# Kernel tuning notes

Measured on AMD Instinct MI355X. Metric: run time of the kernel, lower is better.

Reference implementation:

```python
import jax, jax.numpy as jnp
import numpy as np

B, T, E = 8, 2048, 1024  # batch, seq_len, emb_size (= output_emb_size)


def setup_inputs() -> dict:
    key = jax.random.key(0)
    k1, k2, k3, k4, k5, k6, k7 = jax.random.split(key, 7)
    return {
        "q": jax.random.normal(k1, (B, T, E), jnp.float32),
        "k": jax.random.normal(k2, (B, T, E), jnp.float32),
        "v": jax.random.normal(k3, (B, T, E), jnp.float32),
        "mask": jax.random.randint(k4, (T, T), 0, 2, jnp.int32),
        # nn.Linear weights, stored [out, in] as in torch; applied as x @ W.T
        "Wq": jax.random.normal(k5, (E, E), jnp.float32) / np.sqrt(E),
        "Wk": jax.random.normal(k6, (E, E), jnp.float32) / np.sqrt(E),
        "Wv": jax.random.normal(k7, (E, E), jnp.float32) / np.sqrt(E),
    }


def reference(q, k, v, mask, Wq, Wk, Wv):
    # QKV projections (bias-free Linear): x @ W.T
    query = jnp.einsum("bte,oe->bto", q, Wq)
    key_p = jnp.einsum("bse,oe->bso", k, Wk)
    value = jnp.einsum("bse,oe->bso", v, Wv)
    d = key_p.shape[-1]
    scores = jnp.einsum("bto,bso->bts", query, key_p) / np.sqrt(d).astype(jnp.float32)
    # torch.any(mask): mask is nonzero somewhere -> apply masked_fill(mask==0, -inf)
    scores = jnp.where(mask[None, :, :] == 0, -jnp.inf, scores)
    weights = jax.nn.softmax(scores, axis=-1)
    return jnp.einsum("bts,bso->bto", weights, value)
```

## Files before the change

kernel.cpp:

```cpp
#include <hip/hip_runtime.h>
#include <hip/hip_bf16.h>

typedef __attribute__((ext_vector_type(8))) short short8;
typedef __attribute__((ext_vector_type(8))) unsigned short ushortx8;
typedef __attribute__((ext_vector_type(4))) unsigned short ushortx4;
typedef __attribute__((ext_vector_type(4))) float floatx4;

#define NB 8
#define NT 2048
#define NE 1024

__device__ __forceinline__ unsigned short f2bf(float f){
  unsigned int u = __builtin_bit_cast(unsigned int, f);
  u += 0x7FFFu + ((u >> 16) & 1u);
  return (unsigned short)(u >> 16);
}
__device__ __forceinline__ float bf2f(unsigned short h){
  unsigned int u = ((unsigned int)h) << 16;
  return __builtin_bit_cast(float, u);
}

__device__ __forceinline__ void async16(void* lds, const void* g){
  __builtin_amdgcn_global_load_lds(
      (const __attribute__((address_space(1))) unsigned int*)g,
      (__attribute__((address_space(3))) unsigned int*)lds, 16, 0, 0);
}

__global__ __launch_bounds__(256) void cvt3(const float* __restrict__ a0,
                                            const float* __restrict__ a1,
                                            const float* __restrict__ a2,
                                            unsigned short* __restrict__ out,
                                            int n4_per){
  const float* src = blockIdx.y == 0 ? a0 : (blockIdx.y == 1 ? a1 : a2);
  unsigned short* dst = out + (size_t)blockIdx.y * (size_t)n4_per * 4;
  int i = blockIdx.x * 256 + threadIdx.x;
  if (i < n4_per){
    floatx4 f = ((const floatx4*)src)[i];
    ushortx4 o;
    o.x = f2bf(f.x); o.y = f2bf(f.y); o.z = f2bf(f.z); o.w = f2bf(f.w);
    *(ushortx4*)(dst + (size_t)i * 4) = o;
  }
}

__global__ __launch_bounds__(256) void pack_mask(const int* __restrict__ m,
                                                 unsigned long long* __restrict__ bits){
  int t = blockIdx.x * 256 + threadIdx.x;
  const int4* p = (const int4*)(m + (size_t)t * 64);
  unsigned long long w = 0;
  #pragma unroll
  for (int jj = 0; jj < 16; jj++){
    int4 v = p[jj];
    w |= (unsigned long long)(v.x != 0) << (jj * 4 + 0);
    w |= (unsigned long long)(v.y != 0) << (jj * 4 + 1);
    w |= (unsigned long long)(v.z != 0) << (jj * 4 + 2);
    w |= (unsigned long long)(v.w != 0) << (jj * 4 + 3);
  }
  bits[t] = w;
}

template<int EPI>
__global__ __launch_bounds__(256) void gemm_nt(
    const unsigned short* __restrict__ A, long strideA,
    const unsigned short* __restrict__ B, long strideB,
    void* __restrict__ Out, long strideOutBytes,
    const unsigned long long* __restrict__ mbits,
    int K, int gx, int gy)
{
  __shared__ __attribute__((aligned(16))) unsigned short As[128 * 64];
  __shared__ __attribute__((aligned(16))) unsigned short Bs[128 * 64];
  const int tid = threadIdx.x;
  const int lane = tid & 63, wave = tid >> 6;

  int L = blockIdx.x;
  int xcd = L & 7, t = L >> 3;
  int x = t % gx;
  int strip = xcd + ((t / gx) << 3);
  int y = strip % gy, z = strip / gy;
  const int m0 = y << 7, n0 = x << 7;
  const int Nn = gx << 7;

  const unsigned short* Az = A + (size_t)z * strideA;
  const unsigned short* Bz = B + (size_t)z * strideB;

  const char* gA[4]; const char* gB[4]; int lo[4];
  {
    int s0 = (wave << 8) + lane;
    #pragma unroll
    for (int i = 0; i < 4; i++){
      int s = s0 + (i << 6);
      int row = s >> 3;
      int c = (s & 7) ^ (row & 7);
      lo[i] = s << 4;
      gA[i] = (const char*)(Az + (size_t)(m0 + row) * K) + (c << 4);
      gB[i] = (const char*)(Bz + (size_t)(n0 + row) * K) + (c << 4);
    }
  }
  char* AsB = (char*)As;
  char* BsB = (char*)Bs;

  const int lm = lane & 15, qd = lane >> 4;
  const int wr = (wave >> 1) << 6, wc = (wave & 1) << 6;
  const int sw = lm & 7;
  const char* aB0 = AsB + (wr + lm) * 128 + ((qd ^ sw) << 4);
  const char* aB1 = AsB + (wr + lm) * 128 + (((4 + qd) ^ sw) << 4);
  const char* bB0 = BsB + (wc + lm) * 128 + ((qd ^ sw) << 4);
  const char* bB1 = BsB + (wc + lm) * 128 + (((4 + qd) ^ sw) << 4);

  floatx4 acc[4][4];
  floatx4 zero4 = {0.f, 0.f, 0.f, 0.f};
  #pragma unroll
  for (int a = 0; a < 4; a++)
    #pragma unroll
    for (int b = 0; b < 4; b++) acc[a][b] = zero4;

  for (int kk = 0; kk < K; kk += 64){
    #pragma unroll
    for (int i = 0; i < 4; i++){
      async16(AsB + lo[i], gA[i]);
      async16(BsB + lo[i], gB[i]);
      gA[i] += 128; gB[i] += 128;
    }
    __syncthreads();

    short8 a0[4], a1[4], b0[4], b1[4];
    #pragma unroll
    for (int mi = 0; mi < 4; mi++){
      a0[mi] = *(const short8*)(aB0 + mi * 2048);
      a1[mi] = *(const short8*)(aB1 + mi * 2048);
    }
    #pragma unroll
    for (int ni = 0; ni < 4; ni++){
      b0[ni] = *(const short8*)(bB0 + ni * 2048);
      b1[ni] = *(const short8*)(bB1 + ni * 2048);
    }
    #pragma unroll
    for (int mi = 0; mi < 4; mi++)
      #pragma unroll
      for (int ni = 0; ni < 4; ni++)
        acc[mi][ni] = __builtin_amdgcn_mfma_f32_16x16x32_bf16(a0[mi], b0[ni], acc[mi][ni], 0, 0, 0);
    #pragma unroll
    for (int mi = 0; mi < 4; mi++)
      #pragma unroll
      for (int ni = 0; ni < 4; ni++)
        acc[mi][ni] = __builtin_amdgcn_mfma_f32_16x16x32_bf16(a1[mi], b1[ni], acc[mi][ni], 0, 0, 0);
    __syncthreads();
  }

  char* OutZ = (char*)Out + (size_t)z * strideOutBytes;
  if constexpr (EPI == 1){
    int wcol = (n0 + wc) >> 6;
    #pragma unroll
    for (int mi = 0; mi < 4; mi++){
      #pragma unroll
      for (int i = 0; i < 4; i++){
        int row = m0 + wr + mi * 16 + qd * 4 + i;
        unsigned long long w = mbits[(size_t)row * (NT / 64) + wcol];
        unsigned short* po = (unsigned short*)OutZ + (size_t)row * Nn + n0 + wc;
        #pragma unroll
        for (int ni = 0; ni < 4; ni++){
          float vv = acc[mi][ni][i];
          float s = ((w >> (ni * 16 + lm)) & 1ull) ? vv * 0.03125f : -INFINITY;
          po[ni * 16 + lm] = f2bf(s);
        }
      }
    }
  } else {
    #pragma unroll
    for (int mi = 0; mi < 4; mi++){
      #pragma unroll
      for (int i = 0; i < 4; i++){
        int row = m0 + wr + mi * 16 + qd * 4 + i;
        #pragma unroll
        for (int ni = 0; ni < 4; ni++){
          int col = n0 + wc + ni * 16 + lm;
          float vv = acc[mi][ni][i];
          if constexpr (EPI == 0)
            ((unsigned short*)OutZ)[(size_t)row * Nn + col] = f2bf(vv);
          else
            ((float*)OutZ)[(size_t)row * Nn + col] = vv;
        }
      }
    }
  }
}

__global__ __launch_bounds__(256) void transpose_bf16(const unsigned short* __restrict__ in,
                                                      unsigned short* __restrict__ out,
                                                      int rows, int cols){
  __shared__ __attribute__((aligned(16))) unsigned short tile[64][72];
  const unsigned short* ib = in + (size_t)blockIdx.z * rows * cols;
  unsigned short* ob = out + (size_t)blockIdx.z * rows * cols;
  int r0 = blockIdx.x * 64;
  int c0 = blockIdx.y * 64;
  int tid = threadIdx.x;
  #pragma unroll
  for (int i = 0; i < 2; i++){
    int id = tid + i * 256;
    int r = id >> 3, c = (id & 7) * 8;
    ushortx8 v = *(const ushortx8*)(ib + (size_t)(r0 + r) * cols + c0 + c);
    *(ushortx8*)&tile[r][c] = v;
  }
  __syncthreads();
  #pragma unroll
  for (int i = 0; i < 2; i++){
    int id = tid + i * 256;
    int r = id >> 3, c = (id & 7) * 8;
    ushortx8 v;
    #pragma unroll
    for (int j = 0; j < 8; j++) v[j] = tile[c + j][r];
    *(ushortx8*)(ob + (size_t)(c0 + r) * rows + r0 + c) = v;
  }
}

__global__ __launch_bounds__(256) void softmax_rows(unsigned short* __restrict__ S){
  size_t row = blockIdx.x;
  unsigned short* p = S + row * NT;
  int tid = threadIdx.x;
  ushortx8 v = *(const ushortx8*)(p + tid * 8);
  float f[8];
  #pragma unroll
  for (int j = 0; j < 8; j++) f[j] = bf2f(v[j]);
  float mx = f[0];
  #pragma unroll
  for (int j = 1; j < 8; j++) mx = fmaxf(mx, f[j]);
  #pragma unroll
  for (int off = 32; off > 0; off >>= 1) mx = fmaxf(mx, __shfl_xor(mx, off, 64));
  __shared__ float redm[4], reds[4];
  int lane = tid & 63, wv = tid >> 6;
  if (lane == 0) redm[wv] = mx;
  __syncthreads();
  mx = fmaxf(fmaxf(redm[0], redm[1]), fmaxf(redm[2], redm[3]));
  float e[8]; float se = 0.f;
  #pragma unroll
  for (int j = 0; j < 8; j++){ e[j] = __expf(f[j] - mx); se += e[j]; }
  #pragma unroll
  for (int off = 32; off > 0; off >>= 1) se += __shfl_xor(se, off, 64);
  if (lane == 0) reds[wv] = se;
  __syncthreads();
  se = reds[0] + reds[1] + reds[2] + reds[3];
  float inv = 1.f / se;
  ushortx8 o;
  #pragma unroll
  for (int j = 0; j < 8; j++) o[j] = f2bf(e[j] * inv);
  *(ushortx8*)(p + tid * 8) = o;
}

extern "C" void kernel_launch(void* const* d_in, const int* in_sizes, int n_in,
                              void* d_out, int out_size, void* d_ws, size_t ws_size,
                              hipStream_t stream){
  const float* q  = (const float*)d_in[0];
  const float* k  = (const float*)d_in[1];
  const float* v  = (const float*)d_in[2];
  const int* mask = (const int*)d_in[3];
  const float* Wq = (const float*)d_in[4];
  const float* Wk = (const float*)d_in[5];
  const float* Wv = (const float*)d_in[6];

  const size_t BTE = (size_t)NB * NT * NE;
  unsigned short* ws   = (unsigned short*)d_ws;
  unsigned short* QKVp = ws;
  unsigned short* VpT  = ws + 3 * BTE;
  unsigned short* Sb   = ws + 3 * BTE + BTE;
  unsigned short* Qin  = ws + 3 * BTE;
  unsigned short* Wb   = ws + 3 * BTE + BTE + (size_t)NB * NT * NT;
  unsigned long long* mbits = (unsigned long long*)(Wb + (size_t)3 * NE * NE);

  unsigned short* Qp = QKVp;
  unsigned short* Kp = QKVp + BTE;
  unsigned short* Vp = QKVp + 2 * BTE;

  cvt3<<<dim3(16384, 3), 256, 0, stream>>>(q, k, v, Qin, (int)(BTE / 4));
  cvt3<<<dim3(1024, 3), 256, 0, stream>>>(Wq, Wk, Wv, Wb, NE * NE / 4);
  pack_mask<<<256, 256, 0, stream>>>(mask, mbits);

  gemm_nt<0><<<3072, 256, 0, stream>>>(
      Qin, (long)BTE, Wb, (long)NE * NE,
      QKVp, (long)BTE * 2, nullptr, NE, 8, 128);

  transpose_bf16<<<dim3(32, 16, 8), 256, 0, stream>>>(Vp, VpT, NT, NE);

  gemm_nt<1><<<2048, 256, 0, stream>>>(
      Qp, (long)NT * NE, Kp, (long)NT * NE,
      Sb, (long)NT * NT * 2, mbits, NE, 16, 16);

  softmax_rows<<<dim3(NB * NT), 256, 0, stream>>>(Sb);

  gemm_nt<2><<<1024, 256, 0, stream>>>(
      Sb, (long)NT * NT, VpT, (long)NE * NT,
      d_out, (long)NT * NE * 4, nullptr, NT, 8, 16);
}
```

Measured before the change: 549.4 us.

## Triple-buffer GEMM LDS pipeline with 256x128 tiles and 512-thread blocks

Rewrites the shared GEMM kernel as a three-stage software pipeline. Global-to-LDS async loads for tile k+2 are issued while tile k is computed, and a vmcnt wait plus barrier replaces the two __syncthreads per iteration. Blocks grow to 512 threads covering 256x128 output tiles, so B-tile loads are shared across more waves, and s_setprio is raised around MFMA bursts. This costs much more LDS per block (144KB), which can limit occupancy, and the launch grids are halved to match.

```diff
diff --git a/kernel.cpp b/kernel.cpp
--- a/kernel.cpp
+++ b/kernel.cpp
@@ -59,41 +59,44 @@
 }
 
 template<int EPI>
-__global__ __launch_bounds__(256) void gemm_nt(
+__global__ __launch_bounds__(512, 2) void gemm_nt(
     const unsigned short* __restrict__ A, long strideA,
     const unsigned short* __restrict__ B, long strideB,
     void* __restrict__ Out, long strideOutBytes,
     const unsigned long long* __restrict__ mbits,
     int K, int gx, int gy)
 {
-  __shared__ __attribute__((aligned(16))) unsigned short As[128 * 64];
-  __shared__ __attribute__((aligned(16))) unsigned short Bs[128 * 64];
+  __shared__ __attribute__((aligned(16))) unsigned short As[3 * 256 * 64];
+  __shared__ __attribute__((aligned(16))) unsigned short Bs[3 * 128 * 64];
   const int tid = threadIdx.x;
   const int lane = tid & 63, wave = tid >> 6;
 
   int L = blockIdx.x;
-  int xcd = L & 7, t = L >> 3;
-  int x = t % gx;
-  int strip = xcd + ((t / gx) << 3);
+  int xcd = L & 7, tt = L >> 3;
+  int x = tt % gx;
+  int strip = xcd + ((tt / gx) << 3);
   int y = strip % gy, z = strip / gy;
-  const int m0 = y << 7, n0 = x << 7;
+  const int m0 = y << 8, n0 = x << 7;
   const int Nn = gx << 7;
 
   const unsigned short* Az = A + (size_t)z * strideA;
   const unsigned short* Bz = B + (size_t)z * strideB;
 
-  const char* gA[4]; const char* gB[4]; int lo[4];
-  {
-    int s0 = (wave << 8) + lane;
-    #pragma unroll
-    for (int i = 0; i < 4; i++){
-      int s = s0 + (i << 6);
-      int row = s >> 3;
-      int c = (s & 7) ^ (row & 7);
-      lo[i] = s << 4;
-      gA[i] = (const char*)(Az + (size_t)(m0 + row) * K) + (c << 4);
-      gB[i] = (const char*)(Bz + (size_t)(n0 + row) * K) + (c << 4);
-    }
+  const char* gA[4]; int loA[4];
+  #pragma unroll
+  for (int i = 0; i < 4; i++){
+    int s = (wave << 8) + (i << 6) + lane;
+    int row = s >> 3, c = (s & 7) ^ (row & 7);
+    loA[i] = s << 4;
+    gA[i] = (const char*)(Az + (size_t)(m0 + row) * K) + (c << 4);
+  }
+  const char* gB[2]; int loB[2];
+  #pragma unroll
+  for (int i = 0; i < 2; i++){
+    int s = (wave << 7) + (i << 6) + lane;
+    int row = s >> 3, c = (s & 7) ^ (row & 7);
+    loB[i] = s << 4;
+    gB[i] = (const char*)(Bz + (size_t)(n0 + row) * K) + (c << 4);
   }
   char* AsB = (char*)As;
   char* BsB = (char*)Bs;
@@ -101,10 +104,10 @@
   const int lm = lane & 15, qd = lane >> 4;
   const int wr = (wave >> 1) << 6, wc = (wave & 1) << 6;
   const int sw = lm & 7;
-  const char* aB0 = AsB + (wr + lm) * 128 + ((qd ^ sw) << 4);
-  const char* aB1 = AsB + (wr + lm) * 128 + (((4 + qd) ^ sw) << 4);
-  const char* bB0 = BsB + (wc + lm) * 128 + ((qd ^ sw) << 4);
-  const char* bB1 = BsB + (wc + lm) * 128 + (((4 + qd) ^ sw) << 4);
+  const int offA0 = (wr + lm) * 128 + ((qd ^ sw) << 4);
+  const int offA1 = (wr + lm) * 128 + (((4 + qd) ^ sw) << 4);
+  const int offB0 = (wc + lm) * 128 + ((qd ^ sw) << 4);
+  const int offB1 = (wc + lm) * 128 + (((4 + qd) ^ sw) << 4);
 
   floatx4 acc[4][4];
   floatx4 zero4 = {0.f, 0.f, 0.f, 0.f};
@@ -113,38 +116,60 @@
     #pragma unroll
     for (int b = 0; b < 4; b++) acc[a][b] = zero4;
 
-  for (int kk = 0; kk < K; kk += 64){
-    #pragma unroll
-    for (int i = 0; i < 4; i++){
-      async16(AsB + lo[i], gA[i]);
-      async16(BsB + lo[i], gB[i]);
-      gA[i] += 128; gB[i] += 128;
-    }
-    __syncthreads();
-
+  auto stage = [&](int buf){
+    char* Ad = AsB + (buf << 15);
+    char* Bd = BsB + (buf << 14);
+    #pragma unroll
+    for (int i = 0; i < 4; i++){ async16(Ad + loA[i], gA[i]); gA[i] += 128; }
+    #pragma unroll
+    for (int i = 0; i < 2; i++){ async16(Bd + loB[i], gB[i]); gB[i] += 128; }
+  };
+
+  auto compute = [&](int b){
+    const char* ab = AsB + (b << 15);
+    const char* bb = BsB + (b << 14);
     short8 a0[4], a1[4], b0[4], b1[4];
     #pragma unroll
-    for (int mi = 0; mi < 4; mi++){
-      a0[mi] = *(const short8*)(aB0 + mi * 2048);
-      a1[mi] = *(const short8*)(aB1 + mi * 2048);
-    }
-    #pragma unroll
-    for (int ni = 0; ni < 4; ni++){
-      b0[ni] = *(const short8*)(bB0 + ni * 2048);
-      b1[ni] = *(const short8*)(bB1 + ni * 2048);
-    }
+    for (int mi = 0; mi < 4; mi++) a0[mi] = *(const short8*)(ab + offA0 + mi * 2048);
+    #pragma unroll
+    for (int ni = 0; ni < 4; ni++) b0[ni] = *(const short8*)(bb + offB0 + ni * 2048);
+    __builtin_amdgcn_s_setprio(1);
     #pragma unroll
     for (int mi = 0; mi < 4; mi++)
       #pragma unroll
       for (int ni = 0; ni < 4; ni++)
         acc[mi][ni] = __builtin_amdgcn_mfma_f32_16x16x32_bf16(a0[mi], b0[ni], acc[mi][ni], 0, 0, 0);
+    __builtin_amdgcn_s_setprio(0);
+    #pragma unroll
+    for (int mi = 0; mi < 4; mi++) a1[mi] = *(const short8*)(ab + offA1 + mi * 2048);
+    #pragma unroll
+    for (int ni = 0; ni < 4; ni++) b1[ni] = *(const short8*)(bb + offB1 + ni * 2048);
+    __builtin_amdgcn_s_setprio(1);
     #pragma unroll
     for (int mi = 0; mi < 4; mi++)
       #pragma unroll
       for (int ni = 0; ni < 4; ni++)
         acc[mi][ni] = __builtin_amdgcn_mfma_f32_16x16x32_bf16(a1[mi], b1[ni], acc[mi][ni], 0, 0, 0);
-    __syncthreads();
-  }
+    __builtin_amdgcn_s_setprio(0);
+  };
+
+  const int NK = K >> 6;
+  stage(0);
+  stage(1);
+  asm volatile("s_waitcnt vmcnt(6)\n\ts_barrier" ::: "memory");
+
+  int b = 0, bs = 2;
+  for (int t = 0; t < NK - 2; ++t){
+    stage(bs);
+    compute(b);
+    asm volatile("s_waitcnt vmcnt(6)\n\ts_barrier" ::: "memory");
+    b  = (b  == 2) ? 0 : b  + 1;
+    bs = (bs == 2) ? 0 : bs + 1;
+  }
+  compute(b);
+  asm volatile("s_waitcnt vmcnt(0)\n\ts_barrier" ::: "memory");
+  b = (b == 2) ? 0 : b + 1;
+  compute(b);
 
   char* OutZ = (char*)Out + (size_t)z * strideOutBytes;
   if constexpr (EPI == 1){
@@ -273,19 +298,19 @@
   cvt3<<<dim3(1024, 3), 256, 0, stream>>>(Wq, Wk, Wv, Wb, NE * NE / 4);
   pack_mask<<<256, 256, 0, stream>>>(mask, mbits);
 
-  gemm_nt<0><<<3072, 256, 0, stream>>>(
+  gemm_nt<0><<<1536, 512, 0, stream>>>(
       Qin, (long)BTE, Wb, (long)NE * NE,
-      QKVp, (long)BTE * 2, nullptr, NE, 8, 128);
+      QKVp, (long)BTE * 2, nullptr, NE, 8, 64);
 
   transpose_bf16<<<dim3(32, 16, 8), 256, 0, stream>>>(Vp, VpT, NT, NE);
 
-  gemm_nt<1><<<2048, 256, 0, stream>>>(
+  gemm_nt<1><<<1024, 512, 0, stream>>>(
       Qp, (long)NT * NE, Kp, (long)NT * NE,
-      Sb, (long)NT * NT * 2, mbits, NE, 16, 16);
+      Sb, (long)NT * NT * 2, mbits, NE, 16, 8);
 
   softmax_rows<<<dim3(NB * NT), 256, 0, stream>>>(Sb);
 
-  gemm_nt<2><<<1024, 256, 0, stream>>>(
+  gemm_nt<2><<<512, 512, 0, stream>>>(
       Sb, (long)NT * NT, VpT, (long)NE * NT,
-      d_out, (long)NT * NE * 4, nullptr, NT, 8, 16);
-}
+      d_out, (long)NT * NE * 4, nullptr, NT, 8, 8);
+}
```

Measured after the change: 586.3 us. 1.07x slower.
